# Optimization experiments

Measured on AMD Instinct MI355X. Metric: run time of the kernel, lower is better.

## Reference

```python
import jax, jax.numpy as jnp
import numpy as np

B, N, EMB, NCLS = 4, 4096, 1024, 13

def knn_euclid(x, k):
    # x: (B,C,N); k nearest by squared euclidean distance
    sq = jnp.sum(x * x, axis=1)                        # (B,N)
    inner = jnp.einsum('bcn,bcm->bnm', x, x)           # (B,N,N)
    d = sq[:, :, None] - 2.0 * inner + sq[:, None, :]
    return jax.lax.stop_gradient(jax.lax.top_k(-d, k)[1])   # (B,N,k)

def knn_cosine(x, k):
    xn = x / (jnp.linalg.norm(x, axis=1, keepdims=True) + 1e-8)
    sim = jnp.einsum('bcn,bcm->bnm', xn, xn)           # (B,N,N)
    return jax.lax.stop_gradient(jax.lax.top_k(sim, k)[1])

def edge_conv(x, idx, w0, s0, o0, w1, s1, o1):
    # x: (B,C,N), idx: (B,N,k) -> (B,64,N). Edge feats = concat(x_j - x_i, x_i).
    xt = jnp.transpose(x, (0, 2, 1))                   # (B,N,C)
    nbr = jax.vmap(lambda f, i: f[i])(xt, idx)         # (B,N,k,C)
    ctr = jnp.broadcast_to(xt[:, :, None, :], nbr.shape)
    e = jnp.concatenate([nbr - ctr, ctr], axis=-1)     # (B,N,k,2C)
    h = jax.nn.leaky_relu(jnp.einsum('bnkc,oc->bnko', e, w0) * s0 + o0, 0.2)
    h = jax.nn.leaky_relu(jnp.einsum('bnkc,oc->bnko', h, w1) * s1 + o1, 0.2)
    return jnp.transpose(jnp.max(h, axis=2), (0, 2, 1))  # max over k -> (B,64,N)

def conv1d(x, w):
    return jnp.einsum('bcn,oc->bon', x, w)

def setup_inputs():
    key = jax.random.key(0)
    cnt = [0]
    def nxt():
        cnt[0] += 1
        return jax.random.fold_in(key, cnt[0])
    W = lambda shape: jax.random.normal(nxt(), shape, jnp.float32) * 0.05
    S = lambda n: 1.0 + 0.1 * jax.random.normal(nxt(), (n,), jnp.float32)   # folded BN scale
    O = lambda n: 0.05 * jax.random.normal(nxt(), (n,), jnp.float32)        # folded BN offset / bias
    inp = {'x': jax.random.normal(nxt(), (B, 6, N), jnp.float32)}
    inp.update(w1_0=W((64, 12)), s1_0=S(64), o1_0=O(64), w1_1=W((64, 64)), s1_1=S(64), o1_1=O(64))
    inp.update(w2_0=W((64, 128)), s2_0=S(64), o2_0=O(64), w2_1=W((64, 64)), s2_1=S(64), o2_1=O(64))
    inp.update(w3_0=W((64, 128)), s3_0=S(64), o3_0=O(64), w3_1=W((64, 64)), s3_1=S(64), o3_1=O(64))
    inp.update(w4=W((EMB, 192)), b4=O(EMB))
    inp.update(wf1=W((512, EMB + 192)), sf1=S(512), of1=O(512))
    inp.update(wf2=W((256, 512)), sf2=S(256), of2=O(256))
    inp.update(wf3=W((NCLS, 256)))
    inp['k'] = 20
    return inp

def reference(x, w1_0, s1_0, o1_0, w1_1, s1_1, o1_1,
              w2_0, s2_0, o2_0, w2_1, s2_1, o2_1,
              w3_0, s3_0, o3_0, w3_1, s3_1, o3_1,
              w4, b4, wf1, sf1, of1, wf2, sf2, of2, wf3, k):
    x1 = edge_conv(x, knn_euclid(x, k), w1_0, s1_0, o1_0, w1_1, s1_1, o1_1)
    x2 = edge_conv(x1, knn_cosine(x1, k), w2_0, s2_0, o2_0, w2_1, s2_1, o2_1)
    x3 = edge_conv(x2, knn_cosine(x2, k), w3_0, s3_0, o3_0, w3_1, s3_1, o3_1)
    xc = jnp.concatenate([x1, x2, x3], axis=1)         # (B,192,N)
    x4 = jax.nn.leaky_relu(conv1d(xc, w4) + b4[None, :, None], 0.2)  # (B,EMB,N)
    g = jnp.max(x4, axis=2, keepdims=True)             # global max pool (B,EMB,1)
    g = jnp.broadcast_to(g, (x4.shape[0], x4.shape[1], xc.shape[2]))  # Repeat to N
    x5 = jnp.concatenate([x1, x2, x3, g], axis=1)      # (B,192+EMB,N)
    h = jax.nn.leaky_relu(conv1d(x5, wf1) * sf1[None, :, None] + of1[None, :, None], 0.2)
    h = jax.nn.leaky_relu(conv1d(h, wf2) * sf2[None, :, None] + of2[None, :, None], 0.2)
    return conv1d(h, wf3)                              # (B,NCLS,N)
```

## Files before the change

kernel.cpp:

```cpp
#include <hip/hip_runtime.h>
#include <hip/hip_bf16.h>
#include <float.h>

#define NPTS 4096
#define NB 4
#define KNN 20

typedef __attribute__((ext_vector_type(8))) short short8v;
typedef __attribute__((ext_vector_type(4))) float f32x4;

#define MFMA_B16(acc, a, b) acc = __builtin_amdgcn_mfma_f32_16x16x32_bf16((a), (b), (acc), 0, 0, 0)

__device__ __forceinline__ float lrelu(float x) { return x > 0.f ? x : 0.2f * x; }

__device__ __forceinline__ void atomicMaxF(float* addr, float val) {
    int* ia = (int*)addr;
    int old = *ia;
    while (__int_as_float(old) < val) {
        int assumed = old;
        old = atomicCAS(ia, assumed, __float_as_int(val));
        if (old == assumed) break;
    }
}

__device__ __forceinline__ unsigned bf16rne(float x) {
    unsigned u = __float_as_uint(x);
    return (u + 0x7fffu + ((u >> 16) & 1u)) >> 16;
}

__global__ void k_transp(const float* __restrict__ src, float* __restrict__ dst,
                         int rows, int srcld, int cols) {
    int i = blockIdx.x * 256 + threadIdx.x;
    if (i >= rows * cols) return;
    int r = i % rows, c = i / rows;
    dst[c * rows + r] = src[(size_t)r * srcld + c];
}

__global__ void k_sqnorm(const float* __restrict__ x, float* __restrict__ sq) {
    int i = blockIdx.x * 256 + threadIdx.x;
    int b = i >> 12, n = i & 4095;
    const float* xb = x + b * 6 * NPTS;
    float s = 0.f;
#pragma unroll
    for (int c = 0; c < 6; c++) { float v = xb[c * NPTS + n]; s += v * v; }
    sq[i] = s;
}

__global__ __launch_bounds__(256) void k_knn_euclid(const float* __restrict__ x,
                                                    const float* __restrict__ sq,
                                                    int* __restrict__ idx) {
    int t = threadIdx.x;
    int w = t >> 6, ln = t & 63;
    int qid = blockIdx.x * 4 + w;
    int b = qid >> 12, qn = qid & 4095;
    const float* xb = x + b * 6 * NPTS;
    const float* sqb = sq + b * NPTS;
    float q0 = xb[qn], q1 = xb[NPTS + qn], q2 = xb[2 * NPTS + qn];
    float q3 = xb[3 * NPTS + qn], q4 = xb[4 * NPTS + qn], q5 = xb[5 * NPTS + qn];
    float sqn = sqb[qn];
    float lv = -FLT_MAX; int li = 0x7fffffff;
    float th = -FLT_MAX;
    for (int t0 = 0; t0 < NPTS; t0 += 64) {
        int m = t0 + ln;
        float dot = q0 * xb[m] + q1 * xb[NPTS + m] + q2 * xb[2 * NPTS + m]
                  + q3 * xb[3 * NPTS + m] + q4 * xb[4 * NPTS + m] + q5 * xb[5 * NPTS + m];
        float sv = -(sqn - 2.f * dot + sqb[m]);
        unsigned long long mask = __ballot(sv > th);
        while (mask) {
            int src = __ffsll((unsigned long long)mask) - 1;
            mask &= mask - 1;
            float v = __shfl(sv, src);
            if (!(v > th)) continue;
            int mi = t0 + src;
            float pv = __shfl_up(lv, 1);
            int   pi = __shfl_up(li, 1);
            unsigned long long bm = __ballot(ln < 20 && lv >= v);
            int pos = __popcll(bm);
            if (ln < 20) {
                if (ln == pos) { lv = v; li = mi; }
                else if (ln > pos) { lv = pv; li = pi; }
            }
            th = __shfl(lv, 19);
        }
    }
    if (ln < KNN) idx[qid * KNN + ln] = li;
}

__global__ __launch_bounds__(256) void k_knn_cos(const unsigned short* __restrict__ xs,
                                                 int* __restrict__ idx) {
    __shared__ float simb[16][516];
    int t = threadIdx.x;
    int w = t >> 6, ln = t & 63;
    int b = blockIdx.x >> 8;
    int q0blk = (blockIdx.x & 255) * 16;
    int lp = ln & 15;
    int kg = ln >> 4;
    const unsigned short* xsb = xs + ((size_t)b << 12) * 192;
    const unsigned short* qb = xsb + (size_t)(q0blk + lp) * 192 + kg * 8;
    short8v ah0 = *(const short8v*)(qb);
    short8v ah1 = *(const short8v*)(qb + 32);
    short8v am0 = *(const short8v*)(qb + 64);
    short8v am1 = *(const short8v*)(qb + 96);
    short8v al0 = *(const short8v*)(qb + 128);
    short8v al1 = *(const short8v*)(qb + 160);
    int myq = w * 4;
    float lv[4] = {-FLT_MAX, -FLT_MAX, -FLT_MAX, -FLT_MAX};
    int   li[4] = {0x7fffffff, 0x7fffffff, 0x7fffffff, 0x7fffffff};
    float th[4] = {-FLT_MAX, -FLT_MAX, -FLT_MAX, -FLT_MAX};
    for (int strip = 0; strip < 8; strip++) {
        int c0 = strip * 512 + w * 128;
        for (int tp = 0; tp < 4; tp++) {
            int cand0 = c0 + tp * 32;
            const unsigned short* cb0 = xsb + (size_t)(cand0 + lp) * 192 + kg * 8;
            const unsigned short* cb1 = cb0 + 16 * 192;
            short8v bh0a = *(const short8v*)(cb0);
            short8v bh1a = *(const short8v*)(cb0 + 32);
            short8v bm0a = *(const short8v*)(cb0 + 64);
            short8v bm1a = *(const short8v*)(cb0 + 96);
            short8v bl0a = *(const short8v*)(cb0 + 128);
            short8v bl1a = *(const short8v*)(cb0 + 160);
            short8v bh0b = *(const short8v*)(cb1);
            short8v bh1b = *(const short8v*)(cb1 + 32);
            short8v bm0b = *(const short8v*)(cb1 + 64);
            short8v bm1b = *(const short8v*)(cb1 + 96);
            short8v bl0b = *(const short8v*)(cb1 + 128);
            short8v bl1b = *(const short8v*)(cb1 + 160);
            f32x4 p0 = {0.f, 0.f, 0.f, 0.f}, r0 = {0.f, 0.f, 0.f, 0.f};
            f32x4 p1 = {0.f, 0.f, 0.f, 0.f}, r1 = {0.f, 0.f, 0.f, 0.f};
            MFMA_B16(p0, ah0, bh0a); MFMA_B16(r0, ah1, bh1a);
            MFMA_B16(p1, ah0, bh0b); MFMA_B16(r1, ah1, bh1b);
            MFMA_B16(p0, ah0, bm0a); MFMA_B16(r0, ah1, bm1a);
            MFMA_B16(p1, ah0, bm0b); MFMA_B16(r1, ah1, bm1b);
            MFMA_B16(p0, am0, bh0a); MFMA_B16(r0, am1, bh1a);
            MFMA_B16(p1, am0, bh0b); MFMA_B16(r1, am1, bh1b);
            MFMA_B16(p0, ah0, bl0a); MFMA_B16(r0, ah1, bl1a);
            MFMA_B16(p1, ah0, bl0b); MFMA_B16(r1, ah1, bl1b);
            MFMA_B16(p0, al0, bh0a); MFMA_B16(r0, al1, bh1a);
            MFMA_B16(p1, al0, bh0b); MFMA_B16(r1, al1, bh1b);
            MFMA_B16(p0, am0, bm0a); MFMA_B16(r0, am1, bm1a);
            MFMA_B16(p1, am0, bm0b); MFMA_B16(r1, am1, bm1b);
            f32x4 s0 = p0 + r0;
            f32x4 s1 = p1 + r1;
            int row = kg * 4;
            int colL = w * 128 + tp * 32 + lp;
#pragma unroll
            for (int r = 0; r < 4; r++) {
                simb[row + r][colL] = s0[r];
                simb[row + r][colL + 16] = s1[r];
            }
        }
        __syncthreads();
#pragma unroll
        for (int q = 0; q < 4; q++) {
            for (int j = 0; j < 8; j++) {
                float sv = simb[myq + q][j * 64 + ln];
                int base = strip * 512 + j * 64;
                unsigned long long mask = __ballot(sv > th[q]);
                while (mask) {
                    int src = __ffsll((unsigned long long)mask) - 1;
                    mask &= mask - 1;
                    float v = __shfl(sv, src);
                    if (!(v > th[q])) continue;
                    int mi = base + src;
                    float pv = __shfl_up(lv[q], 1);
                    int   pi = __shfl_up(li[q], 1);
                    unsigned long long bm = __ballot(ln < 20 && lv[q] >= v);
                    int pos = __popcll(bm);
                    if (ln < 20) {
                        if (ln == pos) { lv[q] = v; li[q] = mi; }
                        else if (ln > pos) { lv[q] = pv; li[q] = pi; }
                    }
                    th[q] = __shfl(lv[q], 19);
                }
            }
        }
        __syncthreads();
    }
#pragma unroll
    for (int q = 0; q < 4; q++) {
        if (ln < KNN) {
            int qid = (b << 12) + q0blk + myq + q;
            idx[(size_t)qid * KNN + ln] = li[q];
        }
    }
}

__global__ void k_normalize(const float* __restrict__ xcpm, int coff,
                            unsigned short* __restrict__ xs) {
    int pid = blockIdx.x * 256 + threadIdx.x;
    const float* p = xcpm + (size_t)pid * 192 + coff;
    float s = 0.f;
#pragma unroll
    for (int c4 = 0; c4 < 16; c4++) {
        float4 v = *(const float4*)(p + c4 * 4);
        s += v.x * v.x + v.y * v.y + v.z * v.z + v.w * v.w;
    }
    float inv = 1.f / (sqrtf(s) + 1e-8f);
    unsigned short* q = xs + (size_t)pid * 192;
#pragma unroll
    for (int c4 = 0; c4 < 16; c4++) {
        float4 v = *(const float4*)(p + c4 * 4);
        float f[4] = {v.x * inv, v.y * inv, v.z * inv, v.w * inv};
        unsigned short hh[4], mm[4], ll[4];
#pragma unroll
        for (int j = 0; j < 4; j++) {
            float x = f[j];
            unsigned hb = bf16rne(x);
            float hf = __uint_as_float(hb << 16);
            float r1 = x - hf;
            unsigned mb = bf16rne(r1);
            float mf = __uint_as_float(mb << 16);
            float r2 = r1 - mf;
            unsigned lb = bf16rne(r2);
            hh[j] = (unsigned short)hb; mm[j] = (unsigned short)mb; ll[j] = (unsigned short)lb;
        }
        *(ushort4*)(q + c4 * 4)       = make_ushort4(hh[0], hh[1], hh[2], hh[3]);
        *(ushort4*)(q + 64 + c4 * 4)  = make_ushort4(mm[0], mm[1], mm[2], mm[3]);
        *(ushort4*)(q + 128 + c4 * 4) = make_ushort4(ll[0], ll[1], ll[2], ll[3]);
    }
}

__global__ __launch_bounds__(256) void k_edge1(const float* __restrict__ x,
    const float* __restrict__ w0, const float* __restrict__ s0, const float* __restrict__ o0,
    const float* __restrict__ w1, const float* __restrict__ s1, const float* __restrict__ o1,
    const int* __restrict__ idx, float* __restrict__ xcpm) {
    __shared__ float es[4][16];
    __shared__ float h0s[4][64];
    int t = threadIdx.x;
    int w = t >> 6, o = t & 63;
    int pid = blockIdx.x * 4 + w;
    int b = pid >> 12, n = pid & 4095;
    const float* xb = x + b * 6 * NPTS;
    float w0r[12];
    const float* w0p = w0 + o * 12;
#pragma unroll
    for (int c4 = 0; c4 < 3; c4++) {
        float4 v = *(const float4*)(w0p + c4 * 4);
        w0r[c4 * 4] = v.x; w0r[c4 * 4 + 1] = v.y; w0r[c4 * 4 + 2] = v.z; w0r[c4 * 4 + 3] = v.w;
    }
    float w1r[64];
    const float* w1p = w1 + o * 64;
#pragma unroll
    for (int c4 = 0; c4 < 16; c4++) {
        float4 v = *(const float4*)(w1p + c4 * 4);
        w1r[c4 * 4] = v.x; w1r[c4 * 4 + 1] = v.y; w1r[c4 * 4 + 2] = v.z; w1r[c4 * 4 + 3] = v.w;
    }
    float sv0 = s0[o], ov0 = o0[o], sv1 = s1[o], ov1 = o1[o];
    float cv = 0.f;
    if (o < 6) { cv = xb[o * NPTS + n]; es[w][6 + o] = cv; }
    if (o >= 12 && o < 16) es[w][o] = 0.f;
    float acc = -FLT_MAX;
    const int* ib = idx + pid * KNN;
    for (int kk = 0; kk < KNN; kk++) {
        int j = ib[kk] & 4095;
        if (o < 6) es[w][o] = xb[o * NPTS + j] - cv;
        float h = 0.f;
#pragma unroll
        for (int c4 = 0; c4 < 3; c4++) {
            float4 e4 = *(const float4*)&es[w][c4 * 4];
            h += w0r[c4 * 4] * e4.x + w0r[c4 * 4 + 1] * e4.y + w0r[c4 * 4 + 2] * e4.z + w0r[c4 * 4 + 3] * e4.w;
        }
        h = lrelu(h * sv0 + ov0);
        h0s[w][o] = h;
        float h2 = 0.f;
#pragma unroll
        for (int c4 = 0; c4 < 16; c4++) {
            float4 h4 = *(const float4*)&h0s[w][c4 * 4];
            h2 += w1r[c4 * 4] * h4.x + w1r[c4 * 4 + 1] * h4.y + w1r[c4 * 4 + 2] * h4.z + w1r[c4 * 4 + 3] * h4.w;
        }
        h2 = lrelu(h2 * sv1 + ov1);
        acc = fmaxf(acc, h2);
    }
    xcpm[(size_t)pid * 192 + o] = acc;
}

__global__ __launch_bounds__(256) void k_edge23(const float* __restrict__ xcpm,
    const float* __restrict__ w0, const float* __restrict__ s0, const float* __restrict__ o0,
    const float* __restrict__ w1, const float* __restrict__ s1, const float* __restrict__ o1,
    const int* __restrict__ idx, int ci, int co) {
    __shared__ float cs[4][64];
    __shared__ float es[4][64];
    __shared__ float h0s[4][64];
    int t = threadIdx.x;
    int w = t >> 6, o = t & 63;
    int pid = blockIdx.x * 4 + w;
    int b = pid >> 12;
    float w0r[64];
    const float* w0p = w0 + o * 128;
#pragma unroll
    for (int c4 = 0; c4 < 16; c4++) {
        float4 v = *(const float4*)(w0p + c4 * 4);
        w0r[c4 * 4] = v.x; w0r[c4 * 4 + 1] = v.y; w0r[c4 * 4 + 2] = v.z; w0r[c4 * 4 + 3] = v.w;
    }
    float w1r[64];
    const float* w1p = w1 + o * 64;
#pragma unroll
    for (int c4 = 0; c4 < 16; c4++) {
        float4 v = *(const float4*)(w1p + c4 * 4);
        w1r[c4 * 4] = v.x; w1r[c4 * 4 + 1] = v.y; w1r[c4 * 4 + 2] = v.z; w1r[c4 * 4 + 3] = v.w;
    }
    float sv0 = s0[o], ov0 = o0[o], sv1 = s1[o], ov1 = o1[o];
    float cv = xcpm[(size_t)pid * 192 + ci + o];
    cs[w][o] = cv;
    float h0b = 0.f;
    const float* w0q = w0p + 64;
#pragma unroll
    for (int c4 = 0; c4 < 16; c4++) {
        float4 wv = *(const float4*)(w0q + c4 * 4);
        float4 c4v = *(const float4*)&cs[w][c4 * 4];
        h0b += wv.x * c4v.x + wv.y * c4v.y + wv.z * c4v.z + wv.w * c4v.w;
    }
    float acc = -FLT_MAX;
    const int* ib = idx + pid * KNN;
    int j0 = ib[0] & 4095;
    float nv = xcpm[((size_t)(b * 4096 + j0)) * 192 + ci + o];
    for (int kk = 0; kk < KNN; kk++) {
        float cur = nv;
        if (kk < KNN - 1) {
            int jn = ib[kk + 1] & 4095;
            nv = xcpm[((size_t)(b * 4096 + jn)) * 192 + ci + o];
        }
        es[w][o] = cur - cv;
        float h = h0b;
#pragma unroll
        for (int c4 = 0; c4 < 16; c4++) {
            float4 e4 = *(const float4*)&es[w][c4 * 4];
            h += w0r[c4 * 4] * e4.x + w0r[c4 * 4 + 1] * e4.y + w0r[c4 * 4 + 2] * e4.z + w0r[c4 * 4 + 3] * e4.w;
        }
        h = lrelu(h * sv0 + ov0);
        h0s[w][o] = h;
        float h2 = 0.f;
#pragma unroll
        for (int c4 = 0; c4 < 16; c4++) {
            float4 h4 = *(const float4*)&h0s[w][c4 * 4];
            h2 += w1r[c4 * 4] * h4.x + w1r[c4 * 4 + 1] * h4.y + w1r[c4 * 4 + 2] * h4.z + w1r[c4 * 4 + 3] * h4.w;
        }
        h2 = lrelu(h2 * sv1 + ov1);
        acc = fmaxf(acc, h2);
    }
    float* outp = (float*)xcpm;
    outp[(size_t)pid * 192 + co + o] = acc;
}

__global__ void k_init_g(float* __restrict__ g) {
    g[blockIdx.x * 256 + threadIdx.x] = -FLT_MAX;
}

__global__ __launch_bounds__(256) void k_w4pool(const float* __restrict__ xc,
                                                const float* __restrict__ wT4,
                                                const float* __restrict__ b4,
                                                float* __restrict__ g) {
    __shared__ float xcs[192 * 68];
    int t = threadIdx.x;
    int b = blockIdx.y;
    int n0 = blockIdx.x * 64;
    const float* xb = xc + (size_t)(b * 4096 + n0) * 192;
    for (int i = t; i < 3072; i += 256) {
        int pt = i / 48, c4 = i - pt * 48;
        float4 v = *(const float4*)(xb + pt * 192 + c4 * 4);
        xcs[(c4 * 4 + 0) * 68 + pt] = v.x; xcs[(c4 * 4 + 1) * 68 + pt] = v.y;
        xcs[(c4 * 4 + 2) * 68 + pt] = v.z; xcs[(c4 * 4 + 3) * 68 + pt] = v.w;
    }
    __syncthreads();
    int o0 = (t >> 2) * 16, qd = t & 3;
    float4 bb[4];
#pragma unroll
    for (int k = 0; k < 4; k++) bb[k] = *(const float4*)(b4 + o0 + k * 4);
    float mx[16];
#pragma unroll
    for (int oo = 0; oo < 16; oo++) mx[oo] = -FLT_MAX;
    for (int sub = 0; sub < 4; sub++) {
        int tn0 = sub * 16 + qd * 4;
        float4 acc[16];
#pragma unroll
        for (int oo = 0; oo < 16; oo++) acc[oo] = (float4){0, 0, 0, 0};
        for (int c = 0; c < 192; c++) {
            float4 x4 = *(const float4*)&xcs[c * 68 + tn0];
            const float* wr = wT4 + c * 1024 + o0;
            float4 wq[4];
#pragma unroll
            for (int k = 0; k < 4; k++) wq[k] = *(const float4*)(wr + k * 4);
#pragma unroll
            for (int oo = 0; oo < 16; oo++) {
                float wv = ((const float*)wq)[oo];
                acc[oo].x += wv * x4.x; acc[oo].y += wv * x4.y;
                acc[oo].z += wv * x4.z; acc[oo].w += wv * x4.w;
            }
        }
#pragma unroll
        for (int oo = 0; oo < 16; oo++) {
            float bias = ((const float*)bb)[oo];
            float4 a = acc[oo];
            float h = fmaxf(fmaxf(lrelu(a.x + bias), lrelu(a.y + bias)),
                            fmaxf(lrelu(a.z + bias), lrelu(a.w + bias)));
            mx[oo] = fmaxf(mx[oo], h);
        }
    }
#pragma unroll
    for (int oo = 0; oo < 16; oo++) {
        float v = mx[oo];
        v = fmaxf(v, __shfl_xor(v, 1));
        v = fmaxf(v, __shfl_xor(v, 2));
        if (qd == 0) atomicMaxF(&g[b * 1024 + o0 + oo], v);
    }
}

__global__ __launch_bounds__(256) void k_goff(const float* __restrict__ g,
                                              const float* __restrict__ wf1,
                                              const float* __restrict__ sf1,
                                              const float* __restrict__ of1,
                                              float* __restrict__ goff) {
    int bo = blockIdx.x;
    int b = bo >> 9, o = bo & 511;
    int t = threadIdx.x;
    const float* wr = wf1 + (size_t)o * 1216 + 192;
    const float* gb = g + b * 1024;
    float s = 0.f;
    for (int c = t; c < 1024; c += 256) s += wr[c] * gb[c];
    __shared__ float red[4];
    for (int off = 32; off > 0; off >>= 1) s += __shfl_down(s, off);
    if ((t & 63) == 0) red[t >> 6] = s;
    __syncthreads();
    if (t == 0) {
        float tot = red[0] + red[1] + red[2] + red[3];
        goff[bo] = tot * sf1[o] + of1[o];
    }
}

#define TP 20
__global__ __launch_bounds__(256) void k_tail(const float* __restrict__ xc,
                                              const float* __restrict__ wf1T,
                                              const float* __restrict__ sf1,
                                              const float* __restrict__ goff,
                                              const float* __restrict__ wf2T,
                                              const float* __restrict__ sf2,
                                              const float* __restrict__ of2,
                                              const float* __restrict__ wf3,
                                              float* __restrict__ out) {
    __shared__ float xcs[192 * TP];
    __shared__ float h1s[512 * TP];
    __shared__ float h2s[256 * TP];
    int t = threadIdx.x;
    int b = blockIdx.y;
    int n0 = blockIdx.x * 16;
    const float* xb = xc + (size_t)(b * 4096 + n0) * 192;
    for (int i = t; i < 768; i += 256) {
        int pt = i / 48, c4 = i - pt * 48;
        float4 v = *(const float4*)(xb + pt * 192 + c4 * 4);
        xcs[(c4 * 4 + 0) * TP + pt] = v.x; xcs[(c4 * 4 + 1) * TP + pt] = v.y;
        xcs[(c4 * 4 + 2) * TP + pt] = v.z; xcs[(c4 * 4 + 3) * TP + pt] = v.w;
    }
    __syncthreads();
    {
        int o8 = (t >> 2) * 8, tn0 = (t & 3) * 4;
        float4 acc[8];
#pragma unroll
        for (int oo = 0; oo < 8; oo++) acc[oo] = (float4){0, 0, 0, 0};
        for (int c = 0; c < 192; c++) {
            float4 x4 = *(const float4*)&xcs[c * TP + tn0];
            const float* wr = wf1T + c * 512 + o8;
            float4 w0 = *(const float4*)(wr);
            float4 w1 = *(const float4*)(wr + 4);
            float wq[8] = {w0.x, w0.y, w0.z, w0.w, w1.x, w1.y, w1.z, w1.w};
#pragma unroll
            for (int oo = 0; oo < 8; oo++) {
                acc[oo].x += wq[oo] * x4.x; acc[oo].y += wq[oo] * x4.y;
                acc[oo].z += wq[oo] * x4.z; acc[oo].w += wq[oo] * x4.w;
            }
        }
#pragma unroll
        for (int oo = 0; oo < 8; oo++) {
            int o = o8 + oo;
            float s = sf1[o];
            float gv = goff[b * 512 + o];
            float4 r;
            r.x = lrelu(acc[oo].x * s + gv); r.y = lrelu(acc[oo].y * s + gv);
            r.z = lrelu(acc[oo].z * s + gv); r.w = lrelu(acc[oo].w * s + gv);
            *(float4*)&h1s[o * TP + tn0] = r;
        }
    }
    __syncthreads();
    {
        int o4 = (t >> 2) * 4, tn0 = (t & 3) * 4;
        float4 acc[4];
#pragma unroll
        for (int oo = 0; oo < 4; oo++) acc[oo] = (float4){0, 0, 0, 0};
        for (int c = 0; c < 512; c++) {
            float4 x4 = *(const float4*)&h1s[c * TP + tn0];
            float4 w = *(const float4*)(wf2T + c * 256 + o4);
            float wq[4] = {w.x, w.y, w.z, w.w};
#pragma unroll
            for (int oo = 0; oo < 4; oo++) {
                acc[oo].x += wq[oo] * x4.x; acc[oo].y += wq[oo] * x4.y;
                acc[oo].z += wq[oo] * x4.z; acc[oo].w += wq[oo] * x4.w;
            }
        }
#pragma unroll
        for (int oo = 0; oo < 4; oo++) {
            int o = o4 + oo;
            float s = sf2[o], of = of2[o];
            float4 r;
            r.x = lrelu(acc[oo].x * s + of); r.y = lrelu(acc[oo].y * s + of);
            r.z = lrelu(acc[oo].z * s + of); r.w = lrelu(acc[oo].w * s + of);
            *(float4*)&h2s[o * TP + tn0] = r;
        }
    }
    __syncthreads();
    if (t < 13 * 16) {
        int o = t >> 4, tn = t & 15;
        const float* wr = wf3 + o * 256;
        float acc = 0.f;
        for (int c4 = 0; c4 < 64; c4++) {
            float4 wv = *(const float4*)(wr + c4 * 4);
            acc += wv.x * h2s[(c4 * 4 + 0) * TP + tn] + wv.y * h2s[(c4 * 4 + 1) * TP + tn]
                 + wv.z * h2s[(c4 * 4 + 2) * TP + tn] + wv.w * h2s[(c4 * 4 + 3) * TP + tn];
        }
        out[((size_t)b * 13 + o) * NPTS + n0 + tn] = acc;
    }
}

extern "C" void kernel_launch(void* const* d_in, const int* in_sizes, int n_in,
                              void* d_out, int out_size, void* d_ws, size_t ws_size,
                              hipStream_t stream) {
    const float* x    = (const float*)d_in[0];
    const float* w1_0 = (const float*)d_in[1];
    const float* s1_0 = (const float*)d_in[2];
    const float* o1_0 = (const float*)d_in[3];
    const float* w1_1 = (const float*)d_in[4];
    const float* s1_1 = (const float*)d_in[5];
    const float* o1_1 = (const float*)d_in[6];
    const float* w2_0 = (const float*)d_in[7];
    const float* s2_0 = (const float*)d_in[8];
    const float* o2_0 = (const float*)d_in[9];
    const float* w2_1 = (const float*)d_in[10];
    const float* s2_1 = (const float*)d_in[11];
    const float* o2_1 = (const float*)d_in[12];
    const float* w3_0 = (const float*)d_in[13];
    const float* s3_0 = (const float*)d_in[14];
    const float* o3_0 = (const float*)d_in[15];
    const float* w3_1 = (const float*)d_in[16];
    const float* s3_1 = (const float*)d_in[17];
    const float* o3_1 = (const float*)d_in[18];
    const float* w4   = (const float*)d_in[19];
    const float* b4   = (const float*)d_in[20];
    const float* wf1  = (const float*)d_in[21];
    const float* sf1  = (const float*)d_in[22];
    const float* of1  = (const float*)d_in[23];
    const float* wf2  = (const float*)d_in[24];
    const float* sf2  = (const float*)d_in[25];
    const float* of2  = (const float*)d_in[26];
    const float* wf3  = (const float*)d_in[27];

    float* xcpm = (float*)d_ws;
    float* sq   = xcpm + (size_t)NB * NPTS * 192;
    float* g    = sq + NB * NPTS;
    float* goff = g + NB * 1024;
    int*   idx  = (int*)(goff + NB * 512);
    float* wT4  = (float*)(idx + NB * NPTS * KNN);
    float* wf1T = wT4 + 192 * 1024;
    float* wf2T = wf1T + 192 * 512;
    unsigned short* xs = (unsigned short*)(wf2T + 512 * 256);
    (void)in_sizes; (void)n_in; (void)out_size; (void)ws_size;

    k_transp<<<(1024 * 192 + 255) / 256, 256, 0, stream>>>(w4, wT4, 1024, 192, 192);
    k_transp<<<(512 * 192 + 255) / 256, 256, 0, stream>>>(wf1, wf1T, 512, 1216, 192);
    k_transp<<<(256 * 512 + 255) / 256, 256, 0, stream>>>(wf2, wf2T, 256, 512, 512);
    k_sqnorm<<<NB * NPTS / 256, 256, 0, stream>>>(x, sq);
    k_knn_euclid<<<NB * NPTS / 4, 256, 0, stream>>>(x, sq, idx);
    k_edge1<<<NB * NPTS / 4, 256, 0, stream>>>(x, w1_0, s1_0, o1_0, w1_1, s1_1, o1_1, idx, xcpm);
    k_normalize<<<NB * NPTS / 256, 256, 0, stream>>>(xcpm, 0, xs);
    k_knn_cos<<<NB * NPTS / 16, 256, 0, stream>>>(xs, idx);
    k_edge23<<<NB * NPTS / 4, 256, 0, stream>>>(xcpm, w2_0, s2_0, o2_0, w2_1, s2_1, o2_1, idx, 0, 64);
    k_normalize<<<NB * NPTS / 256, 256, 0, stream>>>(xcpm, 64, xs);
    k_knn_cos<<<NB * NPTS / 16, 256, 0, stream>>>(xs, idx);
    k_edge23<<<NB * NPTS / 4, 256, 0, stream>>>(xcpm, w3_0, s3_0, o3_0, w3_1, s3_1, o3_1, idx, 64, 128);
    k_init_g<<<NB * 1024 / 256, 256, 0, stream>>>(g);
    k_w4pool<<<dim3(NPTS / 64, NB), 256, 0, stream>>>(xcpm, wT4, b4, g);
    k_goff<<<NB * 512, 256, 0, stream>>>(g, wf1, sf1, of1, goff);
    k_tail<<<dim3(NPTS / 16, NB), 256, 0, stream>>>(xcpm, wf1T, sf1, goff, wf2T, sf2, of2, wf3, (float*)d_out);
}
```

Measured before the change: 1.584 ms.

## Replace serial per-candidate top-k insertion with buffered bitonic merge in kNN kernels

```diff
diff --git a/kernel.cpp b/kernel.cpp
--- a/kernel.cpp
+++ b/kernel.cpp
@@ -8,6 +8,7 @@
 
 typedef __attribute__((ext_vector_type(8))) short short8v;
 typedef __attribute__((ext_vector_type(4))) float f32x4;
+typedef unsigned long long u64;
 
 #define MFMA_B16(acc, a, b) acc = __builtin_amdgcn_mfma_f32_16x16x32_bf16((a), (b), (acc), 0, 0, 0)
 
@@ -28,6 +29,37 @@
     return (u + 0x7fffu + ((u >> 16) & 1u)) >> 16;
 }
 
+__device__ __forceinline__ unsigned sortkey_desc(float v) {
+    unsigned u = __float_as_uint(v);
+    unsigned s = (u & 0x80000000u) ? ~u : (u | 0x80000000u);
+    return ~s;
+}
+
+__device__ __forceinline__ u64 bitonic64(u64 e, int ln) {
+#pragma unroll
+    for (int k = 2; k <= 64; k <<= 1) {
+#pragma unroll
+        for (int j = k >> 1; j > 0; j >>= 1) {
+            u64 o = __shfl_xor(e, j);
+            bool keepMin = (((ln & k) == 0) == ((ln & j) == 0));
+            u64 mn = e < o ? e : o;
+            u64 mx = e < o ? o : e;
+            e = keepMin ? mn : mx;
+        }
+    }
+    return e;
+}
+
+__device__ __forceinline__ void topk_merge(u64& topk, unsigned& thk, int& cnt,
+                                           const u64* __restrict__ buf, int ln) {
+    u64 e = (ln < 20) ? topk : ((ln - 20) < cnt ? buf[ln - 20] : ~0ull);
+    e = bitonic64(e, ln);
+    topk = e;
+    u64 e19 = __shfl(e, 19);
+    thk = (unsigned)(e19 >> 32);
+    cnt = 0;
+}
+
 __global__ void k_transp(const float* __restrict__ src, float* __restrict__ dst,
                          int rows, int srcld, int cols) {
     int i = blockIdx.x * 256 + threadIdx.x;
@@ -49,6 +81,7 @@
 __global__ __launch_bounds__(256) void k_knn_euclid(const float* __restrict__ x,
                                                     const float* __restrict__ sq,
                                                     int* __restrict__ idx) {
+    __shared__ u64 ebuf[4][44];
     int t = threadIdx.x;
     int w = t >> 6, ln = t & 63;
     int qid = blockIdx.x * 4 + w;
@@ -58,37 +91,41 @@
     float q0 = xb[qn], q1 = xb[NPTS + qn], q2 = xb[2 * NPTS + qn];
     float q3 = xb[3 * NPTS + qn], q4 = xb[4 * NPTS + qn], q5 = xb[5 * NPTS + qn];
     float sqn = sqb[qn];
-    float lv = -FLT_MAX; int li = 0x7fffffff;
-    float th = -FLT_MAX;
+    u64 topk = ~0ull;
+    unsigned thk = 0xFFFFFFFFu;
+    int cnt = 0;
+    u64* bq = ebuf[w];
     for (int t0 = 0; t0 < NPTS; t0 += 64) {
         int m = t0 + ln;
         float dot = q0 * xb[m] + q1 * xb[NPTS + m] + q2 * xb[2 * NPTS + m]
                   + q3 * xb[3 * NPTS + m] + q4 * xb[4 * NPTS + m] + q5 * xb[5 * NPTS + m];
         float sv = -(sqn - 2.f * dot + sqb[m]);
-        unsigned long long mask = __ballot(sv > th);
-        while (mask) {
-            int src = __ffsll((unsigned long long)mask) - 1;
-            mask &= mask - 1;
-            float v = __shfl(sv, src);
-            if (!(v > th)) continue;
-            int mi = t0 + src;
-            float pv = __shfl_up(lv, 1);
-            int   pi = __shfl_up(li, 1);
-            unsigned long long bm = __ballot(ln < 20 && lv >= v);
-            int pos = __popcll(bm);
-            if (ln < 20) {
-                if (ln == pos) { lv = v; li = mi; }
-                else if (ln > pos) { lv = pv; li = pi; }
-            }
-            th = __shfl(lv, 19);
-        }
-    }
-    if (ln < KNN) idx[qid * KNN + ln] = li;
+        unsigned key = sortkey_desc(sv);
+        bool pass = key < thk;
+        u64 mask = __ballot(pass);
+        if (!mask) continue;
+        u64 key64 = ((u64)key << 32) | (unsigned)m;
+        int cA = __popcll(mask & 0xFFFFFFFFull);
+        int cB = __popcll(mask >> 32);
+        if (cA) {
+            if (cnt + cA > 44) topk_merge(topk, thk, cnt, bq, ln);
+            if (pass && ln < 32) bq[cnt + __popcll(mask & ((1ull << ln) - 1))] = key64;
+            cnt += cA;
+        }
+        if (cB) {
+            if (cnt + cB > 44) topk_merge(topk, thk, cnt, bq, ln);
+            if (pass && ln >= 32) bq[cnt + __popcll((mask >> 32) & ((1ull << (ln - 32)) - 1))] = key64;
+            cnt += cB;
+        }
+    }
+    if (cnt) topk_merge(topk, thk, cnt, bq, ln);
+    if (ln < KNN) idx[qid * KNN + ln] = (int)(topk & 0xFFFFFFFFull);
 }
 
 __global__ __launch_bounds__(256) void k_knn_cos(const unsigned short* __restrict__ xs,
                                                  int* __restrict__ idx) {
     __shared__ float simb[16][516];
+    __shared__ u64 bufp[16][44];
     int t = threadIdx.x;
     int w = t >> 6, ln = t & 63;
     int b = blockIdx.x >> 8;
@@ -104,9 +141,9 @@
     short8v al0 = *(const short8v*)(qb + 128);
     short8v al1 = *(const short8v*)(qb + 160);
     int myq = w * 4;
-    float lv[4] = {-FLT_MAX, -FLT_MAX, -FLT_MAX, -FLT_MAX};
-    int   li[4] = {0x7fffffff, 0x7fffffff, 0x7fffffff, 0x7fffffff};
-    float th[4] = {-FLT_MAX, -FLT_MAX, -FLT_MAX, -FLT_MAX};
+    u64 topk[4] = {~0ull, ~0ull, ~0ull, ~0ull};
+    unsigned thk[4] = {0xFFFFFFFFu, 0xFFFFFFFFu, 0xFFFFFFFFu, 0xFFFFFFFFu};
+    int cnt[4] = {0, 0, 0, 0};
     for (int strip = 0; strip < 8; strip++) {
         int c0 = strip * 512 + w * 128;
         for (int tp = 0; tp < 4; tp++) {
@@ -152,25 +189,25 @@
         __syncthreads();
 #pragma unroll
         for (int q = 0; q < 4; q++) {
+            u64* bq = bufp[myq + q];
             for (int j = 0; j < 8; j++) {
                 float sv = simb[myq + q][j * 64 + ln];
-                int base = strip * 512 + j * 64;
-                unsigned long long mask = __ballot(sv > th[q]);
-                while (mask) {
-                    int src = __ffsll((unsigned long long)mask) - 1;
-                    mask &= mask - 1;
-                    float v = __shfl(sv, src);
-                    if (!(v > th[q])) continue;
-                    int mi = base + src;
-                    float pv = __shfl_up(lv[q], 1);
-                    int   pi = __shfl_up(li[q], 1);
-                    unsigned long long bm = __ballot(ln < 20 && lv[q] >= v);
-                    int pos = __popcll(bm);
-                    if (ln < 20) {
-                        if (ln == pos) { lv[q] = v; li[q] = mi; }
-                        else if (ln > pos) { lv[q] = pv; li[q] = pi; }
-                    }
-                    th[q] = __shfl(lv[q], 19);
+                unsigned key = sortkey_desc(sv);
+                bool pass = key < thk[q];
+                u64 mask = __ballot(pass);
+                if (!mask) continue;
+                u64 key64 = ((u64)key << 32) | (unsigned)(strip * 512 + j * 64 + ln);
+                int cA = __popcll(mask & 0xFFFFFFFFull);
+                int cB = __popcll(mask >> 32);
+                if (cA) {
+                    if (cnt[q] + cA > 44) topk_merge(topk[q], thk[q], cnt[q], bq, ln);
+                    if (pass && ln < 32) bq[cnt[q] + __popcll(mask & ((1ull << ln) - 1))] = key64;
+                    cnt[q] += cA;
+                }
+                if (cB) {
+                    if (cnt[q] + cB > 44) topk_merge(topk[q], thk[q], cnt[q], bq, ln);
+                    if (pass && ln >= 32) bq[cnt[q] + __popcll((mask >> 32) & ((1ull << (ln - 32)) - 1))] = key64;
+                    cnt[q] += cB;
                 }
             }
         }
@@ -178,9 +215,10 @@
     }
 #pragma unroll
     for (int q = 0; q < 4; q++) {
+        if (cnt[q]) topk_merge(topk[q], thk[q], cnt[q], bufp[myq + q], ln);
         if (ln < KNN) {
             int qid = (b << 12) + q0blk + myq + q;
-            idx[(size_t)qid * KNN + ln] = li[q];
+            idx[(size_t)qid * KNN + ln] = (int)(topk[q] & 0xFFFFFFFFull);
         }
     }
 }
```

Result: slower. 1.667 ms (+5.2%).
